# Performance work log

Hardware: AMD Instinct MI355X
Metric: run time of the kernel (lower is better)

## Reference

```python
import jax, jax.numpy as jnp
import numpy as np

NUM_CLASSES = 80
CONF_THRE = 0.2
NMS_THRE = 0.45
MAX_DET = 300   # fixed cap replacing torch's variable-length NMS output (padded + keep mask)
IMG = 640.0


def setup_inputs() -> dict:
    key = jax.random.key(0)
    k1, k2 = jax.random.split(key)
    pred = jax.random.uniform(k1, (32, 8400, 85), dtype=jnp.float32)
    # scale cx,cy,w,h to pixel range so IoU/NMS geometry is realistic
    pred = pred.at[..., :4].multiply(IMG)
    zone = jax.random.uniform(k2, (8, 2), dtype=jnp.float32) * IMG
    return {"prediction": pred, "zone": zone}


def _pairwise_iou(b):
    # b: [B, K, 4] in x1y1x2y2
    area = jnp.clip(b[..., 2] - b[..., 0], 0.0) * jnp.clip(b[..., 3] - b[..., 1], 0.0)
    lt = jnp.maximum(b[:, :, None, :2], b[:, None, :, :2])
    rb = jnp.minimum(b[:, :, None, 2:], b[:, None, :, 2:])
    wh = jnp.clip(rb - lt, 0.0)
    inter = wh[..., 0] * wh[..., 1]
    return inter / (area[:, :, None] + area[:, None, :] - inter + 1e-9)


def _postprocess(prediction):
    # decode cx,cy,w,h -> x1,y1,x2,y2
    xy = prediction[..., :2]
    wh = prediction[..., 2:4]
    boxes = jnp.concatenate([xy - wh * 0.5, xy + wh * 0.5], axis=-1)  # [B,N,4]
    obj = prediction[..., 4]                                           # [B,N]
    cls = prediction[..., 5:5 + NUM_CLASSES]
    class_conf = jnp.max(cls, axis=-1)                                 # [B,N]
    class_pred = jnp.argmax(cls, axis=-1)                              # [B,N]

    # confidence mask (obj * class_conf >= thre); invalid -> -inf so top_k drops them
    nms_score = obj * class_conf
    nms_score = jnp.where(nms_score >= CONF_THRE, nms_score, -jnp.inf)

    s, idx = jax.lax.top_k(nms_score, MAX_DET)                         # [B,K]
    b = jnp.take_along_axis(boxes, idx[..., None], axis=1)             # [B,K,4]

    # class-agnostic greedy NMS on score-sorted boxes (matches torchvision.ops.nms)
    iou = _pairwise_iou(b)                                             # [B,K,K]
    keep = jnp.isfinite(s)                                             # valid (passed conf) entries
    ar = jnp.arange(MAX_DET)
    def body(i, keep):
        sup = keep[:, i][:, None] & (iou[:, i, :] > NMS_THRE) & (ar > i)
        return keep & jnp.logical_not(sup)
    keep = jax.lax.fori_loop(0, MAX_DET, body, keep)

    obj_s = jnp.take_along_axis(obj, idx, axis=1)
    conf_s = jnp.take_along_axis(class_conf, idx, axis=1)
    cls_s = jnp.take_along_axis(class_pred, idx, axis=1).astype(jnp.int32)
    # extract_boxes_scores_and_classes: score = max over columns [obj, class_conf]
    scores = jnp.maximum(obj_s, conf_s)
    return b, scores, cls_s, keep


def _points_inside_zone(px, py, zone):
    # px, py: [B,K]; zone: [Z,2]. Ray-casting parity test (faithful to torch version).
    zr = jnp.roll(zone, shift=1, axis=0)
    xi, yi = zone[:, 0], zone[:, 1]
    xj, yj = zr[:, 0], zr[:, 1]
    pyb = py[..., None]  # [B,K,1] vs [Z]
    pxb = px[..., None]
    gyi = yi > pyb
    gyj = yj > pyb
    gx = (xj - xi) * (pyb - yi) / (yj - yi) + xi
    inter = (gyi != gyj) & (gx > pxb)
    return (jnp.sum(inter.astype(jnp.int32), axis=-1) % 2) > 0


def reference(prediction, zone):
    b, scores, classes, keep = _postprocess(prediction)
    cx = (b[..., 0] + b[..., 2]) * 0.5
    cy = (b[..., 1] + b[..., 3]) * 0.5
    in_zone = _points_inside_zone(cx, cy, zone) & keep
    centers_yx = jnp.stack([cy, cx], axis=-1)                          # [B,K,2]
    boxes_yxyx = jnp.stack([b[..., 1], b[..., 0], b[..., 3], b[..., 2]], axis=-1)
    return boxes_yxyx, in_zone, scores, classes, centers_yx, keep
```

## Files before the change

kernel.cpp:

```cpp
#include <hip/hip_runtime.h>
#include <stdint.h>

typedef unsigned long long ull;

#define NA 8400
#define NB 32
#define KTOP 300
#define NC 80
#define CH 33
#define NBLK 66

#define HIST_OFF 1075200

#define O1 38400
#define O2 48000
#define O3 57600
#define O4 67200
#define O5 86400

__device__ __forceinline__ void g2l16(const void* g, void* l) {
    __builtin_amdgcn_global_load_lds(
        (const __attribute__((address_space(1))) void*)g,
        (__attribute__((address_space(3))) void*)l, 16, 0, 0);
}

__global__ __launch_bounds__(128) void score_kernel(const float* __restrict__ pred,
                                                    uint32_t* __restrict__ keys,
                                                    uint32_t* __restrict__ gHist) {
    __shared__ float sP[128 * 85];
    __shared__ uint32_t sH[4 * 257];
    const int batch = blockIdx.x / NBLK;
    const int blk = blockIdx.x - batch * NBLK;
    const int t = threadIdx.x;
    const int lane = t & 63;
    const int wv = t >> 6;
    const int local0 = blk * 128;
    const int nval = (NA - local0 < 128) ? (NA - local0) : 128;

    for (int i = t; i < 4 * 257; i += 128) sH[i] = 0u;

    const float4* g4 = (const float4*)(pred + ((size_t)batch * NA + local0) * 85);
    float4* l4 = (float4*)sP;
    const int n4 = nval * 85 / 4;
    for (int base = wv * 64; base < n4; base += 128) {
        int idx = base + lane;
        if (idx < n4) g2l16(g4 + idx, l4 + base);
    }
    __syncthreads();

    if (t < nval) {
        const float* p = sP + t * 85;
        float obj = p[4];
        float b0 = p[5], b1 = p[6], b2 = p[7], b3 = p[8];
        #pragma unroll
        for (int c = 4; c < NC; c += 4) {
            b0 = fmaxf(b0, p[5 + c]);
            b1 = fmaxf(b1, p[6 + c]);
            b2 = fmaxf(b2, p[7 + c]);
            b3 = fmaxf(b3, p[8 + c]);
        }
        float best = fmaxf(fmaxf(b0, b1), fmaxf(b2, b3));
        float sc = obj * best;
        uint32_t u = (sc >= 0.2f) ? (__float_as_uint(sc) | 0x80000000u) : 0x007FFFFFu;
        keys[(size_t)batch * NA + local0 + t] = u;
        atomicAdd(&sH[(t >> 5) * 257 + (u >> 24)], 1u);
    }
    __syncthreads();
    uint32_t* gh = gHist + ((size_t)batch * NBLK + blk) * 256;
    for (int bin = t; bin < 256; bin += 128)
        gh[bin] = sH[bin] + sH[257 + bin] + sH[514 + bin] + sH[771 + bin];
}

__global__ __launch_bounds__(256) void topk_nms_kernel(const float* __restrict__ pred,
                                                       const float* __restrict__ zone,
                                                       const uint32_t* __restrict__ keys,
                                                       const uint32_t* __restrict__ gHist,
                                                       float* __restrict__ out) {
    #pragma clang fp contract(off)
    __shared__ uint32_t sKeys[8448];
    __shared__ ull sSel[KTOP];
    __shared__ ull sSorted[KTOP];
    __shared__ uint32_t sH4[4 * 257];
    __shared__ float4 sBox[KTOP];
    __shared__ ull sMask[5 * KTOP];
    __shared__ ull sKeepW[5];
    __shared__ float sZone[16];
    __shared__ uint32_t sWs[8];
    __shared__ uint32_t sBc[2];
    __shared__ int sCnt;

    const int b = blockIdx.x;
    const int t = threadIdx.x;
    const unsigned lane = t & 63;
    const int wv = t >> 6;
    const int sh = wv * 257;

    {
        const float4* k4 = (const float4*)(keys + (size_t)b * NA);
        float4* sk4 = (float4*)sKeys;
        for (int base = wv * 64; base < 2100; base += 256) {
            int idx = base + lane;
            if (idx < 2100) g2l16(k4 + idx, sk4 + base);
        }
    }
    if (t < 48) sKeys[NA + t] = 0u;
    if (t < 16) sZone[t] = zone[t];
    if (t == 0) sCnt = 0;
    __syncthreads();

    uint32_t prefix = 0, r = KTOP;
    for (int round = 0; round < 4; ++round) {
        const int shift = 24 - 8 * round;
        uint32_t h;
        if (round == 0) {
            h = 0;
            const uint32_t* gh = gHist + (size_t)b * NBLK * 256;
            for (int j = 0; j < NBLK; ++j) h += gh[j * 256 + t];
        } else {
            for (int idx = t; idx < 4 * 257; idx += 256) sH4[idx] = 0u;
            __syncthreads();
            const uint32_t pmask = 0xFFFFFFFFu << (shift + 8);
            const uint32_t pval = prefix & pmask;
            for (int s = 0; s < CH; ++s) {
                int e = t * CH + s;
                if (e < NA) {
                    uint32_t k = sKeys[e];
                    if ((k & pmask) == pval)
                        atomicAdd(&sH4[sh + ((k >> shift) & 0xFFu)], 1u);
                }
            }
            __syncthreads();
            h = sH4[t] + sH4[257 + t] + sH4[514 + t] + sH4[771 + t];
        }
        uint32_t val = h;
        #pragma unroll
        for (int d = 1; d < 64; d <<= 1) {
            uint32_t v = __shfl_up(val, d);
            if (lane >= (unsigned)d) val += v;
        }
        if (lane == 63) sWs[wv] = val;
        __syncthreads();
        if (t == 0) {
            uint32_t a = sWs[0], b2 = sWs[1], c = sWs[2];
            sWs[4] = 0; sWs[5] = a; sWs[6] = a + b2; sWs[7] = a + b2 + c;
        }
        __syncthreads();
        uint32_t P = val + sWs[4 + wv];
        uint32_t Total = sWs[7] + sWs[3];
        uint32_t above = Total - P;
        if (above < r && above + h >= r) {
            sBc[0] = prefix | ((uint32_t)t << shift);
            sBc[1] = r - above;
        }
        __syncthreads();
        prefix = sBc[0]; r = sBc[1];
        __syncthreads();
    }
    const uint32_t kth = prefix;
    const uint32_t rem = r;
    const uint32_t cntgt = KTOP - rem;

    {
        uint32_t eqc = 0;
        for (int s = 0; s < CH; ++s) {
            int e = t * CH + s;
            if (e < NA) {
                uint32_t k = sKeys[e];
                if (k > kth) {
                    int p = atomicAdd(&sCnt, 1);
                    sSel[p] = ((ull)k << 32) | (ull)(0xFFFFFFFFu - (uint32_t)e);
                } else if (k == kth) eqc++;
            }
        }
        uint32_t val = eqc;
        #pragma unroll
        for (int d = 1; d < 64; d <<= 1) {
            uint32_t v = __shfl_up(val, d);
            if (lane >= (unsigned)d) val += v;
        }
        if (lane == 63) sWs[wv] = val;
        __syncthreads();
        if (t == 0) {
            uint32_t a = sWs[0], b2 = sWs[1], c = sWs[2];
            sWs[4] = 0; sWs[5] = a; sWs[6] = a + b2; sWs[7] = a + b2 + c;
        }
        __syncthreads();
        uint32_t off0 = val - eqc + sWs[4 + wv];
        for (int s = 0; s < CH; ++s) {
            int e = t * CH + s;
            if (e < NA) {
                uint32_t k = sKeys[e];
                if (k == kth) {
                    if (off0 < rem)
                        sSel[cntgt + off0] = ((ull)k << 32) | (ull)(0xFFFFFFFFu - (uint32_t)e);
                    off0++;
                }
            }
        }
        __syncthreads();
    }

    ull my0 = sSel[t];
    ull my1 = (t < KTOP - 256) ? sSel[256 + t] : 0ull;
    int r0 = 0, r1 = 0;
    for (int j = 0; j < KTOP; ++j) {
        ull v = sSel[j];
        r0 += (v > my0) ? 1 : 0;
        r1 += (v > my1) ? 1 : 0;
    }
    sSorted[r0] = my0;
    if (t < KTOP - 256) sSorted[r1] = my1;
    __syncthreads();

    {
        bool f = ((uint32_t)(sSorted[t] >> 32)) > 0x007FFFFFu;
        ull m = __ballot(f);
        if (lane == 0) sKeepW[wv] = m;
        if (t < 64) {
            bool f2 = (t < KTOP - 256) && (((uint32_t)(sSorted[256 + t] >> 32)) > 0x007FFFFFu);
            ull m2 = __ballot(f2);
            if (t == 0) sKeepW[4] = m2;
        }
    }

    const size_t bo = (size_t)b * KTOP;
    for (int i = t; i < KTOP; i += 256) {
        ull s = sSorted[i];
        uint32_t a = 0xFFFFFFFFu - (uint32_t)(s & 0xFFFFFFFFull);
        const float* p = pred + ((size_t)b * NA + a) * 85;
        float x = p[0], y = p[1], w = p[2], h = p[3], obj = p[4];
        float best = p[5]; int bc = 0;
        for (int c = 1; c < NC; ++c) {
            float v = p[5 + c];
            if (v > best) { best = v; bc = c; }
        }
        float hw = w * 0.5f, hh = h * 0.5f;
        float x1 = x - hw, y1 = y - hh, x2 = x + hw, y2 = y + hh;
        sBox[i] = make_float4(x1, y1, x2, y2);
        ((float4*)out)[bo + i] = make_float4(y1, x1, y2, x2);
        ((float2*)(out + O4))[bo + i] = make_float2((y1 + y2) * 0.5f,
                                                    (x1 + x2) * 0.5f);
        out[O2 + bo + i] = fmaxf(obj, best);
        out[O3 + bo + i] = (float)bc;
    }
    __syncthreads();

    for (int item = t; item < 5 * KTOP; item += 256) {
        int role = item / KTOP;
        int i = item - role * KTOP;
        float4 B = sBox[i];
        float x1 = B.x, y1 = B.y, x2 = B.z, y2 = B.w;
        float ai = fmaxf(x2 - x1, 0.0f) * fmaxf(y2 - y1, 0.0f);
        ull bits = 0ull;
        int j0 = role * 64;
        int jmax = j0 + 64; if (jmax > KTOP) jmax = KTOP;
        int jbeg = (j0 > i + 1) ? j0 : (i + 1);
        for (int j = jbeg; j < jmax; ++j) {
            float4 C = sBox[j];
            float aj = fmaxf(C.z - C.x, 0.0f) * fmaxf(C.w - C.y, 0.0f);
            float iw = fminf(x2, C.z) - fmaxf(x1, C.x); iw = fmaxf(iw, 0.0f);
            float ih = fminf(y2, C.w) - fmaxf(y1, C.y); ih = fmaxf(ih, 0.0f);
            float inter = iw * ih;
            float den = ai + aj;
            den = den - inter;
            den = den + 1e-9f;
            float iou = inter / den;
            if (iou > 0.45f) bits |= (1ull << (j - j0));
        }
        sMask[item] = bits;
    }
    __syncthreads();

    if (t < 64) {
        ull rm[5][5];
        #pragma unroll
        for (int w = 0; w < 5; ++w) {
            int i = w * 64 + t;
            #pragma unroll
            for (int ww = 0; ww < 5; ++ww)
                rm[w][ww] = (i < KTOP) ? sMask[ww * KTOP + i] : 0ull;
        }
        ull kw[5];
        #pragma unroll
        for (int w = 0; w < 5; ++w) kw[w] = sKeepW[w];
        #pragma unroll
        for (int w = 0; w < 5; ++w) {
            ull cur = kw[w];
            while (cur) {
                int ib = __builtin_ctzll(cur);
                ull m0 = __shfl(rm[w][0], ib);
                ull m1 = __shfl(rm[w][1], ib);
                ull m2 = __shfl(rm[w][2], ib);
                ull m3 = __shfl(rm[w][3], ib);
                ull m4 = __shfl(rm[w][4], ib);
                kw[0] &= ~m0; kw[1] &= ~m1; kw[2] &= ~m2; kw[3] &= ~m3; kw[4] &= ~m4;
                ull done = (ib == 63) ? 0ull : (~0ull << (ib + 1));
                cur = kw[w] & done;
            }
        }
        if (t == 0) {
            #pragma unroll
            for (int w = 0; w < 5; ++w) sKeepW[w] = kw[w];
        }
    }
    __syncthreads();

    for (int i = t; i < KTOP; i += 256) {
        int kp = (int)((sKeepW[i >> 6] >> (i & 63)) & 1ull);
        float4 B = sBox[i];
        float cy = (B.y + B.w) * 0.5f;
        float cx = (B.x + B.z) * 0.5f;
        int cnt = 0;
        #pragma unroll
        for (int e = 0; e < 8; ++e) {
            float xi = sZone[2 * e], yi = sZone[2 * e + 1];
            int ep = (e + 7) & 7;
            float xj = sZone[2 * ep], yj = sZone[2 * ep + 1];
            bool gyi = yi > cy, gyj = yj > cy;
            if (gyi != gyj) {
                float gx = (xj - xi) * (cy - yi) / (yj - yi) + xi;
                if (gx > cx) cnt++;
            }
        }
        int inz = (((cnt & 1) != 0) && kp) ? 1 : 0;
        out[O1 + bo + i] = (float)inz;
        out[O5 + bo + i] = (float)kp;
    }
}

extern "C" void kernel_launch(void* const* d_in, const int* in_sizes, int n_in,
                              void* d_out, int out_size, void* d_ws, size_t ws_size,
                              hipStream_t stream) {
    const float* pred = (const float*)d_in[0];
    const float* zone = (const float*)d_in[1];
    float* out = (float*)d_out;
    uint8_t* ws = (uint8_t*)d_ws;
    uint32_t* keys = (uint32_t*)ws;
    uint32_t* gHist = (uint32_t*)(ws + HIST_OFF);

    score_kernel<<<NB * NBLK, 128, 0, stream>>>(pred, keys, gHist);
    topk_nms_kernel<<<NB, 256, 0, stream>>>(pred, zone, keys, gHist, out);
}
```

Baseline: 216.9 us.

## Precompute box and class metadata in score kernel, atomically merge histograms

The score kernel now also computes the argmax class index and writes compact per-anchor xywh and obj/best/class records to workspace. The top-k kernel can then gather two float4s per selected box instead of rescanning the 85-float prediction row, which removes the serial 80-class loop from the single-block-per-batch tail. Per-block histograms are merged with global atomics into one histogram per batch, so round 0 reads one value instead of summing 66. The cost is a large extra workspace write for every anchor (32 bytes each), a memset launch, and atomic contention on the histogram.

```diff
diff --git a/kernel.cpp b/kernel.cpp
--- a/kernel.cpp
+++ b/kernel.cpp
@@ -10,7 +10,9 @@
 #define CH 33
 #define NBLK 66
 
-#define HIST_OFF 1075200
+#define XYWH_OFF 1075200
+#define META_OFF 5376000
+#define HIST_OFF 9676800
 
 #define O1 38400
 #define O2 48000
@@ -26,6 +28,8 @@
 
 __global__ __launch_bounds__(128) void score_kernel(const float* __restrict__ pred,
                                                     uint32_t* __restrict__ keys,
+                                                    float4* __restrict__ xywh4,
+                                                    float4* __restrict__ meta4,
                                                     uint32_t* __restrict__ gHist) {
     __shared__ float sP[128 * 85];
     __shared__ uint32_t sH[4 * 257];
@@ -50,28 +54,41 @@
 
     if (t < nval) {
         const float* p = sP + t * 85;
-        float obj = p[4];
+        float x = p[0], y = p[1], w = p[2], h = p[3], obj = p[4];
         float b0 = p[5], b1 = p[6], b2 = p[7], b3 = p[8];
+        int i0 = 0, i1 = 1, i2 = 2, i3 = 3;
         #pragma unroll
         for (int c = 4; c < NC; c += 4) {
-            b0 = fmaxf(b0, p[5 + c]);
-            b1 = fmaxf(b1, p[6 + c]);
-            b2 = fmaxf(b2, p[7 + c]);
-            b3 = fmaxf(b3, p[8 + c]);
+            float v0 = p[5 + c], v1 = p[6 + c], v2 = p[7 + c], v3 = p[8 + c];
+            if (v0 > b0) { b0 = v0; i0 = c; }
+            if (v1 > b1) { b1 = v1; i1 = c + 1; }
+            if (v2 > b2) { b2 = v2; i2 = c + 2; }
+            if (v3 > b3) { b3 = v3; i3 = c + 3; }
         }
         float best = fmaxf(fmaxf(b0, b1), fmaxf(b2, b3));
+        int bi = 0x7FFFFFFF;
+        if (b3 == best) bi = i3;
+        if (b2 == best && i2 < bi) bi = i2;
+        if (b1 == best && i1 < bi) bi = i1;
+        if (b0 == best && i0 < bi) bi = i0;
         float sc = obj * best;
         uint32_t u = (sc >= 0.2f) ? (__float_as_uint(sc) | 0x80000000u) : 0x007FFFFFu;
-        keys[(size_t)batch * NA + local0 + t] = u;
+        const size_t gi = (size_t)batch * NA + local0 + t;
+        keys[gi] = u;
+        xywh4[gi] = make_float4(x, y, w, h);
+        meta4[gi] = make_float4(obj, best, (float)bi, 0.0f);
         atomicAdd(&sH[(t >> 5) * 257 + (u >> 24)], 1u);
     }
     __syncthreads();
-    uint32_t* gh = gHist + ((size_t)batch * NBLK + blk) * 256;
-    for (int bin = t; bin < 256; bin += 128)
-        gh[bin] = sH[bin] + sH[257 + bin] + sH[514 + bin] + sH[771 + bin];
+    uint32_t* gh = gHist + (size_t)batch * 256;
+    for (int bin = t; bin < 256; bin += 128) {
+        uint32_t v = sH[bin] + sH[257 + bin] + sH[514 + bin] + sH[771 + bin];
+        if (v) atomicAdd(&gh[bin], v);
+    }
 }
 
-__global__ __launch_bounds__(256) void topk_nms_kernel(const float* __restrict__ pred,
+__global__ __launch_bounds__(256) void topk_nms_kernel(const float4* __restrict__ xywh4,
+                                                       const float4* __restrict__ meta4,
                                                        const float* __restrict__ zone,
                                                        const uint32_t* __restrict__ keys,
                                                        const uint32_t* __restrict__ gHist,
@@ -113,9 +130,7 @@
         const int shift = 24 - 8 * round;
         uint32_t h;
         if (round == 0) {
-            h = 0;
-            const uint32_t* gh = gHist + (size_t)b * NBLK * 256;
-            for (int j = 0; j < NBLK; ++j) h += gh[j * 256 + t];
+            h = gHist[(size_t)b * 256 + t];
         } else {
             for (int idx = t; idx < 4 * 257; idx += 256) sH4[idx] = 0u;
             __syncthreads();
@@ -227,21 +242,17 @@
     for (int i = t; i < KTOP; i += 256) {
         ull s = sSorted[i];
         uint32_t a = 0xFFFFFFFFu - (uint32_t)(s & 0xFFFFFFFFull);
-        const float* p = pred + ((size_t)b * NA + a) * 85;
-        float x = p[0], y = p[1], w = p[2], h = p[3], obj = p[4];
-        float best = p[5]; int bc = 0;
-        for (int c = 1; c < NC; ++c) {
-            float v = p[5 + c];
-            if (v > best) { best = v; bc = c; }
-        }
-        float hw = w * 0.5f, hh = h * 0.5f;
-        float x1 = x - hw, y1 = y - hh, x2 = x + hw, y2 = y + hh;
+        size_t g = (size_t)b * NA + a;
+        float4 xw = xywh4[g];
+        float4 mt = meta4[g];
+        float hw = xw.z * 0.5f, hh = xw.w * 0.5f;
+        float x1 = xw.x - hw, y1 = xw.y - hh, x2 = xw.x + hw, y2 = xw.y + hh;
         sBox[i] = make_float4(x1, y1, x2, y2);
         ((float4*)out)[bo + i] = make_float4(y1, x1, y2, x2);
         ((float2*)(out + O4))[bo + i] = make_float2((y1 + y2) * 0.5f,
                                                     (x1 + x2) * 0.5f);
-        out[O2 + bo + i] = fmaxf(obj, best);
-        out[O3 + bo + i] = (float)bc;
+        out[O2 + bo + i] = fmaxf(mt.x, mt.y);
+        out[O3 + bo + i] = mt.z;
     }
     __syncthreads();
 
@@ -336,8 +347,11 @@
     float* out = (float*)d_out;
     uint8_t* ws = (uint8_t*)d_ws;
     uint32_t* keys = (uint32_t*)ws;
+    float4* xywh4 = (float4*)(ws + XYWH_OFF);
+    float4* meta4 = (float4*)(ws + META_OFF);
     uint32_t* gHist = (uint32_t*)(ws + HIST_OFF);
 
-    score_kernel<<<NB * NBLK, 128, 0, stream>>>(pred, keys, gHist);
-    topk_nms_kernel<<<NB, 256, 0, stream>>>(pred, zone, keys, gHist, out);
+    hipMemsetAsync(gHist, 0, NB * 256 * sizeof(uint32_t), stream);
+    score_kernel<<<NB * NBLK, 128, 0, stream>>>(pred, keys, xywh4, meta4, gHist);
+    topk_nms_kernel<<<NB, 256, 0, stream>>>(xywh4, meta4, zone, keys, gHist, out);
 }
```

Result: faster. 205.5 us (-5.3%).
